# Kernel tuning notes

Measured on AMD Instinct MI355X. Metric: run time of the kernel, lower is better.

## Reference

```python
import jax, jax.numpy as jnp
import numpy as np

COL = 14
NJ = 14
SIGMA = 1.0
RADIUS = int(4.0 * SIGMA + 0.5)  # scipy gaussian_filter default truncate=4.0 -> radius 4

def _gaussian_matrix():
    # 1D operator matrix G[y_out, y_src] of scipy.ndimage.gaussian_filter with
    # sigma=1, mode='reflect' (== numpy 'symmetric' padding) on a length-COL axis.
    w = np.exp(-0.5 * (np.arange(-RADIUS, RADIUS + 1) / SIGMA) ** 2)
    w = w / w.sum()
    eye_p = np.pad(np.eye(COL), ((RADIUS, RADIUS), (0, 0)), mode='symmetric')
    G = sum(w[k] * eye_p[k:k + COL] for k in range(2 * RADIUS + 1))
    return jnp.asarray(G.astype(np.float32))

G_MAT = _gaussian_matrix()

def setup_inputs():
    key = jax.random.key(0)
    k1, k2, k3 = jax.random.split(key, 3)
    B = 8192
    out = jax.random.normal(k1, (B, 3 * NJ, COL, COL), dtype=jnp.float32)
    t = jax.random.uniform(k2, (B, NJ, 2), dtype=jnp.float32)  # normalized coords in [0,1)
    v = jax.random.randint(k3, (B, NJ, 1), 0, 2).astype(jnp.float32)
    v = jnp.tile(v, (1, 1, 2))  # visibility flag duplicated over (x,y) channels
    return {"out": out, "t": t, "v": v}

def _forward(out, t, v):
    B = out.shape[0]
    scale = 1.0 / COL
    h = out[:, :NJ]          # [B,NJ,COL,COL] heatmaps
    o = out[:, NJ:]          # [B,2*NJ,COL,COL] offset maps (x offsets then y offsets)
    # per-joint argmax over flattened grid (first-occurrence, same as torch .max)
    idx = jnp.argmax(h.reshape(B, NJ, COL * COL), axis=-1)    # [B,NJ]
    yc = idx // COL
    xc = idx % COL
    # gather offsets at the argmax location
    o_flat = o.reshape(B, 2 * NJ, COL * COL)
    ox = jnp.take_along_axis(o_flat[:, :NJ], idx[:, :, None], axis=2)[..., 0]
    oy = jnp.take_along_axis(o_flat[:, NJ:], idx[:, :, None], axis=2)[..., 0]
    x_pred = jnp.stack([(ox + xc.astype(out.dtype)) * scale,
                        (oy + yc.astype(out.dtype)) * scale], axis=-1)  # [B,NJ,2]
    # gaussian target construction (constant w.r.t. the network output)
    ti = (t * COL).astype(jnp.int32)      # int() truncation; t >= 0
    xi, yi = ti[..., 0], ti[..., 1]
    inb = (xi >= 0) & (xi <= COL - 1) & (yi >= 0) & (yi <= COL - 1)
    vis = v[..., 0].astype(jnp.int32) == 1
    scat = vis & inb                       # joints that receive a gaussian target
    v_eff = jnp.where((vis & ~inb)[..., None], 0.0, v)  # out-of-bounds visible -> zeroed
    # gaussian-filtered one-hot == outer(G[:,yi], G[:,xi]) (separable splat)
    gy = G_MAT.T[jnp.clip(yi, 0, COL - 1)]   # [B,NJ,COL]
    gx = G_MAT.T[jnp.clip(xi, 0, COL - 1)]   # [B,NJ,COL]
    tt = gy[..., :, None] * gx[..., None, :]  # [B,NJ,COL,COL]
    mn = tt.min(axis=(2, 3), keepdims=True)
    mx = tt.max(axis=(2, 3), keepdims=True)
    tt = jnp.where(scat[..., None, None], (tt - mn) / (mx - mn), 0.0)
    # heatmap loss; original zeroes only ROW 0 of the map for invisible joints
    diff1 = h - tt
    vis_eff = (v_eff[..., 0].astype(jnp.int32) == 1)
    diff1 = diff1.at[:, :, 0, :].set(diff1[:, :, 0, :] * vis_eff[..., None].astype(diff1.dtype))
    cnt = jnp.sum(vis_eff.astype(jnp.float32))
    d1 = jnp.sum(diff1 * diff1) / cnt
    # coordinate loss, masked by (possibly updated) visibility
    diff2 = (x_pred - t) * v_eff
    n2 = v_eff.sum() / 2.0
    d2 = jnp.sum(diff2 * diff2) / n2
    return d1 + d2

def reference(out, t, v):
    return _forward(out, t, v)
```

## Files before the change

### kernel.cpp

```cpp
#include <hip/hip_runtime.h>


#define COL 14
#define NJ 14
#define CELLS (COL * COL)
#define THREADS 256
#define WPB (THREADS / 64)
#define BLOCKS 2048
#define MAXI 16
#define NEGINF -3.402823466e38f

__global__ __launch_bounds__(THREADS)
void mse3_main(const float* __restrict__ outp, const float* __restrict__ tp,
               const float* __restrict__ vp, double* __restrict__ partial, int npair)
{
    __shared__ float Gs[CELLS];
    __shared__ float cminS[COL], cmaxS[COL];
    __shared__ double part[WPB][4];

    const int tid = threadIdx.x;

    if (tid < CELLS) {
        const double wraw[9] = {3.3546262790251185e-4, 1.1108996538242306e-2,
                                1.353352832366127e-1,  6.065306597126334e-1, 1.0,
                                6.065306597126334e-1,  1.353352832366127e-1,
                                1.1108996538242306e-2, 3.3546262790251185e-4};
        const double Z = 2.5066208042307818;
        int gi = tid / COL;
        int gj = tid - COL * gi;
        double a = 0.0;
#pragma unroll
        for (int k = 0; k < 9; ++k) {
            int r = gi + k;
            int m = (r < 4) ? (3 - r) : ((r < 18) ? (r - 4) : (31 - r));
            if (m == gj) a += wraw[k] / Z;
        }
        Gs[tid] = (float)a;
    }
    __syncthreads();
    if (tid < COL) {
        float mn = Gs[tid], mx = mn;
        for (int r = 1; r < COL; ++r) {
            float g = Gs[r * COL + tid];
            mn = fminf(mn, g);
            mx = fmaxf(mx, g);
        }
        cminS[tid] = mn;
        cmaxS[tid] = mx;
    }
    __syncthreads();

    const int lane   = tid & 63;
    const int wv     = tid >> 6;
    const int gwave  = blockIdx.x * WPB + wv;
    const int nwaves = BLOCKS * WPB;

    float s1 = 0.0f, s2 = 0.0f, cnt = 0.0f, n2 = 0.0f;

    for (int pbase = gwave; pbase < npair; pbase += nwaves * MAXI) {
        const int m = min(MAXI, (npair - pbase + nwaves - 1) / nwaves);

        int packreg = 0;
        float tvx = 0.f, tvy = 0.f, vvx = 0.f, vvy = 0.f;
        if (lane < m) {
            int p = pbase + lane * nwaves;
            float2 tv = reinterpret_cast<const float2*>(tp)[p];
            float2 vv = reinterpret_cast<const float2*>(vp)[p];
            tvx = tv.x; tvy = tv.y; vvx = vv.x; vvy = vv.y;
            int xi = (int)(tv.x * 14.0f);
            int yi = (int)(tv.y * 14.0f);
            bool inb    = (xi >= 0) && (xi <= COL - 1) && (yi >= 0) && (yi <= COL - 1);
            bool vis    = ((int)vv.x == 1);
            bool scat   = vis && inb;
            bool zeroed = vis && !inb;
            float ve0   = zeroed ? 0.0f : vv.x;
            bool vise   = ((int)ve0 == 1);
            int xic = min(max(xi, 0), COL - 1);
            int yic = min(max(yi, 0), COL - 1);
            packreg = xic | (yic << 4) | (scat ? 256 : 0) | (vise ? 512 : 0)
                          | (zeroed ? 1024 : 0);
        }

        float4 hv_next = make_float4(0.f, 0.f, 0.f, 0.f);
        if (lane < 49) {
            int b = pbase / NJ, j = pbase - NJ * b;
            hv_next = reinterpret_cast<const float4*>(
                outp + ((size_t)b * (3 * NJ) + j) * CELLS)[lane];
        }

        int myidx = 0;
        for (int i = 0; i < m; ++i) {
            float4 hv = hv_next;
            if (i + 1 < m && lane < 49) {
                int p = pbase + (i + 1) * nwaves;
                int b = p / NJ, j = p - NJ * b;
                hv_next = reinterpret_cast<const float4*>(
                    outp + ((size_t)b * (3 * NJ) + j) * CELLS)[lane];
            }
            const int pk = __shfl(packreg, i, 64);
            const int xic = pk & 15;
            const int yic = (pk >> 4) & 15;
            const bool scat = (pk & 256) != 0;
            const bool vise = (pk & 512) != 0;

            float best = NEGINF;
            int bidx = 0;
            if (lane < 49) {
                best = hv.x; bidx = 4 * lane;
                if (hv.y > best) { best = hv.y; bidx = 4 * lane + 1; }
                if (hv.z > best) { best = hv.z; bidx = 4 * lane + 2; }
                if (hv.w > best) { best = hv.w; bidx = 4 * lane + 3; }
            }
#pragma unroll
            for (int off = 32; off >= 1; off >>= 1) {
                float ov = __shfl_down(best, off, 64);
                int   oi = __shfl_down(bidx, off, 64);
                if (ov > best || (ov == best && oi < bidx)) { best = ov; bidx = oi; }
            }
            const int idxb = __shfl(bidx, 0, 64);
            if (lane == i) myidx = idxb;

            if (lane < 49) {
                float h4[4] = {hv.x, hv.y, hv.z, hv.w};
                int y = (4 * lane) / COL;
                int x = 4 * lane - COL * y;
                if (scat) {
                    float mn  = cminS[yic] * cminS[xic];
                    float mx  = cmaxS[yic] * cmaxS[xic];
                    float inv = 1.0f / (mx - mn);
#pragma unroll
                    for (int c = 0; c < 4; ++c) {
                        float tt = (Gs[y * COL + yic] * Gs[x * COL + xic] - mn) * inv;
                        float d = h4[c] - tt;
                        if (y == 0 && !vise) d = 0.0f;
                        s1 += d * d;
                        ++x; if (x == COL) { x = 0; ++y; }
                    }
                } else {
#pragma unroll
                    for (int c = 0; c < 4; ++c) {
                        float d = h4[c];
                        if (y == 0 && !vise) d = 0.0f;
                        s1 += d * d;
                        ++x; if (x == COL) { x = 0; ++y; }
                    }
                }
            }
        }

        if (lane < m) {
            int p = pbase + lane * nwaves;
            int b = p / NJ, j = p - NJ * b;
            const float* base = outp + (size_t)b * (3 * NJ) * CELLS;
            float ox = base[(size_t)(NJ + j) * CELLS + myidx];
            float oy = base[(size_t)(2 * NJ + j) * CELLS + myidx];
            bool zeroed = (packreg & 1024) != 0;
            bool vise   = (packreg & 512) != 0;
            float ve0 = zeroed ? 0.0f : vvx;
            float ve1 = zeroed ? 0.0f : vvy;
            int yc = myidx / COL;
            int xc = myidx - COL * yc;
            const float SC = (float)(1.0 / 14.0);
            float dx = (ox + (float)xc) * SC - tvx; dx *= ve0;
            float dy = (oy + (float)yc) * SC - tvy; dy *= ve1;
            s2 += dx * dx + dy * dy;
            if (vise) cnt += 1.0f;
            n2 += ve0 + ve1;
        }
    }

#pragma unroll
    for (int off = 32; off >= 1; off >>= 1) {
        s1  += __shfl_down(s1,  off, 64);
        s2  += __shfl_down(s2,  off, 64);
        cnt += __shfl_down(cnt, off, 64);
        n2  += __shfl_down(n2,  off, 64);
    }
    if (lane == 0) {
        part[wv][0] = (double)s1;
        part[wv][1] = (double)s2;
        part[wv][2] = (double)cnt;
        part[wv][3] = (double)n2;
    }
    __syncthreads();
    if (tid == 0) {
        double a0 = 0, a1 = 0, a2 = 0, a3 = 0;
        for (int i = 0; i < WPB; ++i) {
            a0 += part[i][0]; a1 += part[i][1];
            a2 += part[i][2]; a3 += part[i][3];
        }
        double* o = partial + (size_t)blockIdx.x * 4;
        o[0] = a0; o[1] = a1; o[2] = a2; o[3] = a3;
    }
}

__global__ __launch_bounds__(256)
void mse3_final(const double* __restrict__ partial, float* __restrict__ o)
{
    __shared__ double p2[4][4];
    double a0 = 0, a1 = 0, a2 = 0, a3 = 0;
    for (int b = threadIdx.x; b < BLOCKS; b += 256) {
        const double* q = partial + (size_t)b * 4;
        a0 += q[0]; a1 += q[1]; a2 += q[2]; a3 += q[3];
    }
#pragma unroll
    for (int off = 32; off >= 1; off >>= 1) {
        a0 += __shfl_down(a0, off, 64);
        a1 += __shfl_down(a1, off, 64);
        a2 += __shfl_down(a2, off, 64);
        a3 += __shfl_down(a3, off, 64);
    }
    const int lane = threadIdx.x & 63, wv = threadIdx.x >> 6;
    if (lane == 0) { p2[wv][0] = a0; p2[wv][1] = a1; p2[wv][2] = a2; p2[wv][3] = a3; }
    __syncthreads();
    if (threadIdx.x == 0) {
        double s1 = 0, s2 = 0, cn = 0, nn = 0;
        for (int i = 0; i < 4; ++i) {
            s1 += p2[i][0]; s2 += p2[i][1]; cn += p2[i][2]; nn += p2[i][3];
        }
        o[0] = (float)(s1 / cn + s2 / (0.5 * nn));
    }
}

extern "C" void kernel_launch(void* const* d_in, const int* in_sizes, int n_in,
                              void* d_out, int out_size, void* d_ws, size_t ws_size,
                              hipStream_t stream)
{
    const float* outp = (const float*)d_in[0];
    const float* tp   = (const float*)d_in[1];
    const float* vp   = (const float*)d_in[2];
    double* partial = (double*)d_ws;

    const int B = in_sizes[0] / (3 * NJ * CELLS);
    const int npair = B * NJ;

    mse3_main<<<BLOCKS, THREADS, 0, stream>>>(outp, tp, vp, partial, npair);
    mse3_final<<<1, 256, 0, stream>>>(partial, (float*)d_out);
}
```

Measured before the change: 330.9 us.

## Map one heatmap per thread instead of one per wavefront

Each thread now handles one (batch, joint) pair. It streams that pair's 196 heatmap cells with float4 loads, computing argmax and the target loss in registers, so the cross-lane shuffle reductions of the old wave-per-heatmap scheme go away. Blocks are 64 threads with one per 64 pairs, and the final reduction takes the block count as a parameter. The cost is uncoalesced strided loads: each lane reads a separate 784-byte row, plus higher register pressure from the fully unrolled 49-iteration loop and the gx/gy arrays.

```diff
diff --git a/kernel.cpp b/kernel.cpp
--- a/kernel.cpp
+++ b/kernel.cpp
@@ -4,30 +4,35 @@
 #define COL 14
 #define NJ 14
 #define CELLS (COL * COL)
-#define THREADS 256
-#define WPB (THREADS / 64)
-#define BLOCKS 2048
-#define MAXI 16
 #define NEGINF -3.402823466e38f
 
-__global__ __launch_bounds__(THREADS)
+#define CELL1(CIDX, HVAL)                                             \
+    {                                                                 \
+        const int   cc = (CIDX);                                      \
+        const float hh = (HVAL);                                      \
+        if (hh > best) { best = hh; bidx = cc; }                      \
+        float tt = (gy[cc / COL] * gx[cc % COL] - mnv) * inv;         \
+        float dd = hh - tt;                                           \
+        if (cc < COL) dd = vise ? dd : 0.0f;                          \
+        s1 += dd * dd;                                                \
+    }
+
+__global__ __launch_bounds__(64)
 void mse3_main(const float* __restrict__ outp, const float* __restrict__ tp,
                const float* __restrict__ vp, double* __restrict__ partial, int npair)
 {
     __shared__ float Gs[CELLS];
     __shared__ float cminS[COL], cmaxS[COL];
-    __shared__ double part[WPB][4];
+    const int lane = threadIdx.x;
 
-    const int tid = threadIdx.x;
-
-    if (tid < CELLS) {
+    for (int cell = lane; cell < CELLS; cell += 64) {
         const double wraw[9] = {3.3546262790251185e-4, 1.1108996538242306e-2,
                                 1.353352832366127e-1,  6.065306597126334e-1, 1.0,
                                 6.065306597126334e-1,  1.353352832366127e-1,
                                 1.1108996538242306e-2, 3.3546262790251185e-4};
         const double Z = 2.5066208042307818;
-        int gi = tid / COL;
-        int gj = tid - COL * gi;
+        int gi = cell / COL;
+        int gj = cell - COL * gi;
         double a = 0.0;
 #pragma unroll
         for (int k = 0; k < 9; ++k) {
@@ -35,171 +40,98 @@
             int m = (r < 4) ? (3 - r) : ((r < 18) ? (r - 4) : (31 - r));
             if (m == gj) a += wraw[k] / Z;
         }
-        Gs[tid] = (float)a;
+        Gs[cell] = (float)a;
     }
     __syncthreads();
-    if (tid < COL) {
-        float mn = Gs[tid], mx = mn;
+    if (lane < COL) {
+        float mn = Gs[lane], mx = mn;
         for (int r = 1; r < COL; ++r) {
-            float g = Gs[r * COL + tid];
+            float g = Gs[r * COL + lane];
             mn = fminf(mn, g);
             mx = fmaxf(mx, g);
         }
-        cminS[tid] = mn;
-        cmaxS[tid] = mx;
+        cminS[lane] = mn;
+        cmaxS[lane] = mx;
     }
     __syncthreads();
 
-    const int lane   = tid & 63;
-    const int wv     = tid >> 6;
-    const int gwave  = blockIdx.x * WPB + wv;
-    const int nwaves = BLOCKS * WPB;
-
+    const int p = blockIdx.x * 64 + lane;
     float s1 = 0.0f, s2 = 0.0f, cnt = 0.0f, n2 = 0.0f;
 
-    for (int pbase = gwave; pbase < npair; pbase += nwaves * MAXI) {
-        const int m = min(MAXI, (npair - pbase + nwaves - 1) / nwaves);
+    if (p < npair) {
+        float2 tv = reinterpret_cast<const float2*>(tp)[p];
+        float2 vv = reinterpret_cast<const float2*>(vp)[p];
+        int xi = (int)(tv.x * 14.0f);
+        int yi = (int)(tv.y * 14.0f);
+        bool inb    = (xi >= 0) && (xi <= COL - 1) && (yi >= 0) && (yi <= COL - 1);
+        bool vis    = ((int)vv.x == 1);
+        bool scat   = vis && inb;
+        bool zeroed = vis && !inb;
+        float ve0   = zeroed ? 0.0f : vv.x;
+        float ve1   = zeroed ? 0.0f : vv.y;
+        bool  vise  = ((int)ve0 == 1);
+        int xic = min(max(xi, 0), COL - 1);
+        int yic = min(max(yi, 0), COL - 1);
 
-        int packreg = 0;
-        float tvx = 0.f, tvy = 0.f, vvx = 0.f, vvy = 0.f;
-        if (lane < m) {
-            int p = pbase + lane * nwaves;
-            float2 tv = reinterpret_cast<const float2*>(tp)[p];
-            float2 vv = reinterpret_cast<const float2*>(vp)[p];
-            tvx = tv.x; tvy = tv.y; vvx = vv.x; vvy = vv.y;
-            int xi = (int)(tv.x * 14.0f);
-            int yi = (int)(tv.y * 14.0f);
-            bool inb    = (xi >= 0) && (xi <= COL - 1) && (yi >= 0) && (yi <= COL - 1);
-            bool vis    = ((int)vv.x == 1);
-            bool scat   = vis && inb;
-            bool zeroed = vis && !inb;
-            float ve0   = zeroed ? 0.0f : vv.x;
-            bool vise   = ((int)ve0 == 1);
-            int xic = min(max(xi, 0), COL - 1);
-            int yic = min(max(yi, 0), COL - 1);
-            packreg = xic | (yic << 4) | (scat ? 256 : 0) | (vise ? 512 : 0)
-                          | (zeroed ? 1024 : 0);
+        float gy[COL], gx[COL];
+#pragma unroll
+        for (int r = 0; r < COL; ++r) {
+            gy[r] = Gs[r * COL + yic];
+            gx[r] = Gs[r * COL + xic];
+        }
+        float mnq = cminS[yic] * cminS[xic];
+        float mxq = cmaxS[yic] * cmaxS[xic];
+        float mnv = scat ? mnq : 0.0f;
+        float inv = scat ? 1.0f / (mxq - mnq) : 0.0f;
+
+        int b = p / NJ, j = p - NJ * b;
+        const float4* h4p = reinterpret_cast<const float4*>(
+            outp + ((size_t)b * (3 * NJ) + j) * CELLS);
+
+        float best = NEGINF;
+        int   bidx = 0;
+#pragma unroll
+        for (int k = 0; k < 49; ++k) {
+            float4 hq = h4p[k];
+            CELL1(4 * k + 0, hq.x);
+            CELL1(4 * k + 1, hq.y);
+            CELL1(4 * k + 2, hq.z);
+            CELL1(4 * k + 3, hq.w);
         }
 
-        float4 hv_next = make_float4(0.f, 0.f, 0.f, 0.f);
-        if (lane < 49) {
-            int b = pbase / NJ, j = pbase - NJ * b;
-            hv_next = reinterpret_cast<const float4*>(
-                outp + ((size_t)b * (3 * NJ) + j) * CELLS)[lane];
-        }
-
-        int myidx = 0;
-        for (int i = 0; i < m; ++i) {
-            float4 hv = hv_next;
-            if (i + 1 < m && lane < 49) {
-                int p = pbase + (i + 1) * nwaves;
-                int b = p / NJ, j = p - NJ * b;
-                hv_next = reinterpret_cast<const float4*>(
-                    outp + ((size_t)b * (3 * NJ) + j) * CELLS)[lane];
-            }
-            const int pk = __shfl(packreg, i, 64);
-            const int xic = pk & 15;
-            const int yic = (pk >> 4) & 15;
-            const bool scat = (pk & 256) != 0;
-            const bool vise = (pk & 512) != 0;
-
-            float best = NEGINF;
-            int bidx = 0;
-            if (lane < 49) {
-                best = hv.x; bidx = 4 * lane;
-                if (hv.y > best) { best = hv.y; bidx = 4 * lane + 1; }
-                if (hv.z > best) { best = hv.z; bidx = 4 * lane + 2; }
-                if (hv.w > best) { best = hv.w; bidx = 4 * lane + 3; }
-            }
-#pragma unroll
-            for (int off = 32; off >= 1; off >>= 1) {
-                float ov = __shfl_down(best, off, 64);
-                int   oi = __shfl_down(bidx, off, 64);
-                if (ov > best || (ov == best && oi < bidx)) { best = ov; bidx = oi; }
-            }
-            const int idxb = __shfl(bidx, 0, 64);
-            if (lane == i) myidx = idxb;
-
-            if (lane < 49) {
-                float h4[4] = {hv.x, hv.y, hv.z, hv.w};
-                int y = (4 * lane) / COL;
-                int x = 4 * lane - COL * y;
-                if (scat) {
-                    float mn  = cminS[yic] * cminS[xic];
-                    float mx  = cmaxS[yic] * cmaxS[xic];
-                    float inv = 1.0f / (mx - mn);
-#pragma unroll
-                    for (int c = 0; c < 4; ++c) {
-                        float tt = (Gs[y * COL + yic] * Gs[x * COL + xic] - mn) * inv;
-                        float d = h4[c] - tt;
-                        if (y == 0 && !vise) d = 0.0f;
-                        s1 += d * d;
-                        ++x; if (x == COL) { x = 0; ++y; }
-                    }
-                } else {
-#pragma unroll
-                    for (int c = 0; c < 4; ++c) {
-                        float d = h4[c];
-                        if (y == 0 && !vise) d = 0.0f;
-                        s1 += d * d;
-                        ++x; if (x == COL) { x = 0; ++y; }
-                    }
-                }
-            }
-        }
-
-        if (lane < m) {
-            int p = pbase + lane * nwaves;
-            int b = p / NJ, j = p - NJ * b;
-            const float* base = outp + (size_t)b * (3 * NJ) * CELLS;
-            float ox = base[(size_t)(NJ + j) * CELLS + myidx];
-            float oy = base[(size_t)(2 * NJ + j) * CELLS + myidx];
-            bool zeroed = (packreg & 1024) != 0;
-            bool vise   = (packreg & 512) != 0;
-            float ve0 = zeroed ? 0.0f : vvx;
-            float ve1 = zeroed ? 0.0f : vvy;
-            int yc = myidx / COL;
-            int xc = myidx - COL * yc;
-            const float SC = (float)(1.0 / 14.0);
-            float dx = (ox + (float)xc) * SC - tvx; dx *= ve0;
-            float dy = (oy + (float)yc) * SC - tvy; dy *= ve1;
-            s2 += dx * dx + dy * dy;
-            if (vise) cnt += 1.0f;
-            n2 += ve0 + ve1;
-        }
+        const float* ob = outp + (size_t)b * (3 * NJ) * CELLS;
+        float ox = ob[(size_t)(NJ + j) * CELLS + bidx];
+        float oy = ob[(size_t)(2 * NJ + j) * CELLS + bidx];
+        int yc = bidx / COL;
+        int xc = bidx - COL * yc;
+        const float SC = (float)(1.0 / 14.0);
+        float dx = (ox + (float)xc) * SC - tv.x; dx *= ve0;
+        float dy = (oy + (float)yc) * SC - tv.y; dy *= ve1;
+        s2  = dx * dx + dy * dy;
+        cnt = vise ? 1.0f : 0.0f;
+        n2  = ve0 + ve1;
     }
 
+    double r0 = (double)s1, r1 = (double)s2, r2 = (double)cnt, r3 = (double)n2;
 #pragma unroll
     for (int off = 32; off >= 1; off >>= 1) {
-        s1  += __shfl_down(s1,  off, 64);
-        s2  += __shfl_down(s2,  off, 64);
-        cnt += __shfl_down(cnt, off, 64);
-        n2  += __shfl_down(n2,  off, 64);
+        r0 += __shfl_down(r0, off, 64);
+        r1 += __shfl_down(r1, off, 64);
+        r2 += __shfl_down(r2, off, 64);
+        r3 += __shfl_down(r3, off, 64);
     }
     if (lane == 0) {
-        part[wv][0] = (double)s1;
-        part[wv][1] = (double)s2;
-        part[wv][2] = (double)cnt;
-        part[wv][3] = (double)n2;
-    }
-    __syncthreads();
-    if (tid == 0) {
-        double a0 = 0, a1 = 0, a2 = 0, a3 = 0;
-        for (int i = 0; i < WPB; ++i) {
-            a0 += part[i][0]; a1 += part[i][1];
-            a2 += part[i][2]; a3 += part[i][3];
-        }
         double* o = partial + (size_t)blockIdx.x * 4;
-        o[0] = a0; o[1] = a1; o[2] = a2; o[3] = a3;
+        o[0] = r0; o[1] = r1; o[2] = r2; o[3] = r3;
     }
 }
 
 __global__ __launch_bounds__(256)
-void mse3_final(const double* __restrict__ partial, float* __restrict__ o)
+void mse3_final(const double* __restrict__ partial, float* __restrict__ o, int nblk)
 {
     __shared__ double p2[4][4];
     double a0 = 0, a1 = 0, a2 = 0, a3 = 0;
-    for (int b = threadIdx.x; b < BLOCKS; b += 256) {
+    for (int b = threadIdx.x; b < nblk; b += 256) {
         const double* q = partial + (size_t)b * 4;
         a0 += q[0]; a1 += q[1]; a2 += q[2]; a3 += q[3];
     }
@@ -233,7 +165,8 @@
 
     const int B = in_sizes[0] / (3 * NJ * CELLS);
     const int npair = B * NJ;
+    const int nblk = (npair + 63) / 64;
 
-    mse3_main<<<BLOCKS, THREADS, 0, stream>>>(outp, tp, vp, partial, npair);
-    mse3_final<<<1, 256, 0, stream>>>(partial, (float*)d_out);
+    mse3_main<<<nblk, 64, 0, stream>>>(outp, tp, vp, partial, npair);
+    mse3_final<<<1, 256, 0, stream>>>(partial, (float*)d_out, nblk);
 }
```

After: 334.3 us. Within noise of the previous version (+1.0%).
